# Kernel tuning notes

Measured on AMD Instinct MI355X. Metric: run time of the kernel, lower is better.

## Reference

```python
import jax, jax.numpy as jnp
import numpy as np

IH, IW = 14, 14
NUM_HEADS = 16
HEAD_DIMS = 32
INP_DIMS = 512
B = 128


def make_relative_position_index(ih, iw):
    coords = np.stack(np.meshgrid(np.arange(ih), np.arange(iw), indexing='ij'))  # [2, ih, iw]
    cf = coords.reshape(2, -1)  # [2, n]
    rel = cf[:, :, None] - cf[:, None, :]  # [2, n, n]
    rel = rel.transpose(1, 2, 0)  # [n, n, 2]
    rel[:, :, 0] += ih - 1
    rel[:, :, 1] += iw - 1
    rel[:, :, 0] *= 2 * iw - 1
    return rel.sum(-1).astype(np.int64)  # [n, n]


def setup_inputs() -> dict:
    key = jax.random.key(0)
    k1, k2, k3, k4, k5 = jax.random.split(key, 5)
    n = IH * IW
    inner = NUM_HEADS * HEAD_DIMS
    x = jax.random.normal(k1, (B, n, INP_DIMS), dtype=jnp.float32)
    qkv_w = jax.random.normal(k2, (INP_DIMS, 3 * inner), dtype=jnp.float32) * 0.02
    rel_bias_table = jax.random.normal(k3, ((2 * IH - 1) * (2 * IW - 1), NUM_HEADS), dtype=jnp.float32) * 0.02
    proj_w = jax.random.normal(k4, (inner, INP_DIMS), dtype=jnp.float32) * 0.02
    proj_b = jax.random.normal(k5, (INP_DIMS,), dtype=jnp.float32) * 0.02
    rel_pos_index = jnp.asarray(make_relative_position_index(IH, IW))
    return {"x": x, "qkv_w": qkv_w, "rel_bias_table": rel_bias_table,
            "proj_w": proj_w, "proj_b": proj_b, "rel_pos_index": rel_pos_index}


def reference(x, qkv_w, rel_bias_table, proj_w, proj_b, rel_pos_index):
    b, n, c = x.shape
    h, hd = NUM_HEADS, HEAD_DIMS
    scale = (INP_DIMS // NUM_HEADS) ** (-0.5)
    qkv = x @ qkv_w  # [b, n, 3*h*hd]
    qkv = qkv.reshape(b, n, 3, h, hd).transpose(2, 0, 3, 1, 4)  # [3, b, h, n, hd]
    q, k, v = qkv[0] * scale, qkv[1], qkv[2]
    attn = jnp.einsum('bhqd,bhkd->bhqk', q, k)  # [b, h, n, n]
    # gather relative position bias: [n*n, h] -> [h, n, n]
    bias = rel_bias_table[rel_pos_index.reshape(-1)].reshape(n, n, h).transpose(2, 0, 1)
    attn = jax.nn.softmax(attn + bias[None], axis=-1)
    out = jnp.einsum('bhqk,bhkd->bhqd', attn, v)  # [b, h, n, hd]
    out = out.transpose(0, 2, 1, 3).reshape(b, n, h * hd)
    return out @ proj_w + proj_b
```

## Files before the change

kernel.cpp:

```cpp
#include <hip/hip_runtime.h>

#define NTOK 196
#define QPAD 208
#define KP 208
#define PSTR 232
#define VKP 208

typedef __attribute__((ext_vector_type(8))) short short8;
typedef __attribute__((ext_vector_type(4))) short short4_t;
typedef __attribute__((ext_vector_type(4))) float float4_t;

__device__ __forceinline__ short f2bf(float f) {
  unsigned u = __float_as_uint(f);
  u = (u + 0x7fffu + ((u >> 16) & 1u)) >> 16;
  return (short)u;
}

__global__ __launch_bounds__(256) void fill_kernel(float* __restrict__ out,
                                                   int n) {
  int i = blockIdx.x * 256 + threadIdx.x;
  if (i < n) out[i] = 1000.0f;
}

__device__ __forceinline__ void transpose_body(const float* __restrict__ in,
                                               short* __restrict__ out, int R,
                                               int C, int bx, int by,
                                               float (*tile)[65]) {
  int c0 = bx * 64, r0 = by * 64;
  int tc = threadIdx.x & 63, tr = threadIdx.x >> 6;
#pragma unroll
  for (int s = 0; s < 16; s++) {
    int r = s * 4 + tr;
    tile[r][tc] = in[(r0 + r) * C + c0 + tc];
  }
  __syncthreads();
#pragma unroll
  for (int s = 0; s < 16; s++) {
    int i = s * 4 + tr;
    out[(c0 + i) * R + r0 + tc] = f2bf(tile[tc][i]);
  }
}

__global__ __launch_bounds__(256) void prep_kernel(
    const float* __restrict__ qkv_w, const float* __restrict__ proj_w,
    const float* __restrict__ table, const int* __restrict__ rpi,
    const float* __restrict__ x, short* __restrict__ wt1,
    short* __restrict__ wt2, float* __restrict__ bias, short* __restrict__ vb,
    short* __restrict__ xb, int do_vpad) {
  __shared__ float tile[64][65];
  int blk = blockIdx.x;
  if (blk < 192) {
    transpose_body(qkv_w, wt1, 512, 1536, blk % 24, blk / 24, tile);
  } else if (blk < 256) {
    int i = blk - 192;
    transpose_body(proj_w, wt2, 512, 512, i % 8, i / 8, tile);
  } else if (blk < 2960) {
    int idx = (blk - 256) * 256 + threadIdx.x;
    int h = idx / (QPAD * KP);
    int rem = idx % (QPAD * KP);
    int q = rem / KP, k = rem % KP;
    float v = 0.f;
    if (q < NTOK && k < NTOK)
      v = table[rpi[q * NTOK + k] * 16 + h] * 1.4426950408889634f;
    bias[idx] = v;
  } else if (blk < 3728) {
    if (do_vpad) {
      int i = (blk - 2960) * 256 + threadIdx.x;
      int row = i / 3, g = i - 3 * (i / 3);
      short4_t z = {0, 0, 0, 0};
      *(short4_t*)&vb[row * VKP + 196 + g * 4] = z;
    }
  } else {
    int i = ((blk - 3728) * 256 + threadIdx.x) * 8;
    float4_t a = *(const float4_t*)&x[i];
    float4_t b = *(const float4_t*)&x[i + 4];
    short8 v;
    v[0] = f2bf(a[0]); v[1] = f2bf(a[1]); v[2] = f2bf(a[2]); v[3] = f2bf(a[3]);
    v[4] = f2bf(b[0]); v[5] = f2bf(b[1]); v[6] = f2bf(b[2]); v[7] = f2bf(b[3]);
    *(short8*)&xb[i] = v;
  }
}

__device__ __forceinline__ void gemm_tile(const short* __restrict__ A,
                                          const short* __restrict__ B, int K,
                                          int m0, int n0, short (*As)[72],
                                          short (*Bs)[72], float4_t acc[4][4]) {
  int tid = threadIdx.x;
  int lane = tid & 63, wave = tid >> 6;
  int quad = lane >> 4, l16 = lane & 15;
  int wm = (wave >> 1) * 64, wn = (wave & 1) * 64;
  int srow = tid >> 3, scol = (tid & 7) * 8;
  for (int k0 = 0; k0 < K; k0 += 64) {
#pragma unroll
    for (int i = 0; i < 4; i++) {
      int r = srow + i * 32;
      *(short8*)&As[r][scol] = *(const short8*)&A[(m0 + r) * K + k0 + scol];
      *(short8*)&Bs[r][scol] = *(const short8*)&B[(n0 + r) * K + k0 + scol];
    }
    __syncthreads();
#pragma unroll
    for (int ks = 0; ks < 2; ks++) {
      short8 af[4], bfr[4];
#pragma unroll
      for (int i = 0; i < 4; i++) {
        af[i] = *(short8*)&As[wm + i * 16 + l16][ks * 32 + quad * 8];
        bfr[i] = *(short8*)&Bs[wn + i * 16 + l16][ks * 32 + quad * 8];
      }
#pragma unroll
      for (int mi = 0; mi < 4; mi++)
#pragma unroll
        for (int ni = 0; ni < 4; ni++)
          acc[mi][ni] = __builtin_amdgcn_mfma_f32_16x16x32_bf16(
              af[mi], bfr[ni], acc[mi][ni], 0, 0, 0);
    }
    __syncthreads();
  }
}

__global__ __launch_bounds__(256) void qkv_gemm(
    const short* __restrict__ xb, const short* __restrict__ wt1,
    short* __restrict__ qb, short* __restrict__ kb, short* __restrict__ vb) {
  __shared__ __align__(16) short As[128][72];
  __shared__ __align__(16) short Bs[128][72];
  float4_t acc[4][4];
  float4_t z = {0.f, 0.f, 0.f, 0.f};
#pragma unroll
  for (int i = 0; i < 4; i++)
#pragma unroll
    for (int j = 0; j < 4; j++) acc[i][j] = z;
  int lin = blockIdx.x + blockIdx.y * 12;
  int xcd = lin & 7, loc = lin >> 3;
  int nl = xcd * 294 + loc;
  int bx = nl % 12, by = nl / 12;
  int m0 = by * 128, n0 = bx * 128;
  gemm_tile(xb, wt1, 512, m0, n0, As, Bs, acc);
  int lane = threadIdx.x & 63, wave = threadIdx.x >> 6;
  int quad = lane >> 4, l16 = lane & 15;
  int wm = (wave >> 1) * 64, wn = (wave & 1) * 64;
  const float qscale = 0.17677669529663687f * 1.4426950408889634f;
#pragma unroll
  for (int mi = 0; mi < 4; mi++)
#pragma unroll
    for (int ni = 0; ni < 4; ni++) {
      int colg = n0 + wn + ni * 16 + l16;
      int s = colg >> 9, rem = colg & 511;
      int h = rem >> 5, d = rem & 31;
      int rowg0 = m0 + wm + mi * 16 + quad * 4;
      if (s == 2) {
        int b = rowg0 / NTOK, nt = rowg0 - b * NTOK;
        short4_t v4;
        v4[0] = f2bf(acc[mi][ni][0]);
        v4[1] = f2bf(acc[mi][ni][1]);
        v4[2] = f2bf(acc[mi][ni][2]);
        v4[3] = f2bf(acc[mi][ni][3]);
        *(short4_t*)&vb[((b * 16 + h) * 32 + d) * VKP + nt] = v4;
      } else {
#pragma unroll
        for (int r = 0; r < 4; r++) {
          int rowg = rowg0 + r;
          int b = rowg / NTOK, n = rowg - b * NTOK;
          int off = ((b * 16 + h) * QPAD + n) * 32 + d;
          if (s == 0)
            qb[off] = f2bf(acc[mi][ni][r] * qscale);
          else
            kb[off] = f2bf(acc[mi][ni][r]);
        }
      }
    }
}

__global__ __launch_bounds__(256) void attn_kernel(
    const short* __restrict__ qb, const short* __restrict__ kb,
    const short* __restrict__ vb, const float* __restrict__ bias,
    short* __restrict__ aout) {
  __shared__ __align__(16) short vT[32][PSTR];
  __shared__ __align__(16) short P[4][16][PSTR];
  int bh = blockIdx.x, b = bh >> 4, h = bh & 15;
  int tid = threadIdx.x, wave = tid >> 6, lane = tid & 63;
  int quad = lane >> 4, l16 = lane & 15;
  int base_row = b * NTOK;
  const short* vsrc = vb + bh * 32 * VKP;
  for (int i = tid; i < 32 * 26; i += 256) {
    int d = i / 26, c = (i - d * 26) * 8;
    *(short8*)&vT[d][c] = *(const short8*)&vsrc[d * VKP + c];
  }
  short8 z8 = {0, 0, 0, 0, 0, 0, 0, 0};
  if (tid < 96) {
    int d = tid / 3, c = 208 + (tid - d * 3) * 8;
    *(short8*)&vT[d][c] = z8;
  }
  __syncthreads();
  short8 kfr[13];
#pragma unroll
  for (int kt = 0; kt < 13; kt++)
    kfr[kt] = *(const short8*)&kb[(bh * QPAD + kt * 16 + l16) * 32 + quad * 8];
  float4_t z4 = {0.f, 0.f, 0.f, 0.f};
  for (int i2 = 0; i2 < 4; i2++) {
    bool active = (i2 < 3) || (wave == 0);
    if (!active) break;
    int qt = (i2 < 3) ? (wave + 4 * i2) : 12;
    int qr0 = qt * 16;
    short8 qf = *(const short8*)&qb[(bh * QPAD + qr0 + l16) * 32 + quad * 8];
    float4_t s[13];
#pragma unroll
    for (int kt = 0; kt < 13; kt++)
      s[kt] = __builtin_amdgcn_mfma_f32_16x16x32_bf16(qf, kfr[kt], z4, 0, 0, 0);
    const float* brow = bias + (h * QPAD + qr0 + quad * 4) * KP;
#pragma unroll
    for (int kt = 0; kt < 13; kt++) {
      int col = kt * 16 + l16;
#pragma unroll
      for (int r = 0; r < 4; r++) s[kt][r] += brow[r * KP + col];
    }
    if (l16 >= 4) {
#pragma unroll
      for (int r = 0; r < 4; r++) s[12][r] = -1e30f;
    }
    float invr[4];
#pragma unroll
    for (int r = 0; r < 4; r++) {
      float m = s[0][r];
#pragma unroll
      for (int kt = 1; kt < 13; kt++) m = fmaxf(m, s[kt][r]);
      m = fmaxf(m, __shfl_xor(m, 8, 16));
      m = fmaxf(m, __shfl_xor(m, 4, 16));
      m = fmaxf(m, __shfl_xor(m, 2, 16));
      m = fmaxf(m, __shfl_xor(m, 1, 16));
      float sum = 0.f;
#pragma unroll
      for (int kt = 0; kt < 13; kt++) {
        float p = exp2f(s[kt][r] - m);
        s[kt][r] = p;
        sum += p;
      }
      sum += __shfl_xor(sum, 8, 16);
      sum += __shfl_xor(sum, 4, 16);
      sum += __shfl_xor(sum, 2, 16);
      sum += __shfl_xor(sum, 1, 16);
      invr[r] = 1.f / sum;
      short* prow = &P[wave][quad * 4 + r][0];
#pragma unroll
      for (int kt = 0; kt < 13; kt++)
        prow[kt * 16 + l16] = f2bf(s[kt][r]);
      prow[208 + l16] = 0;
    }
    float4_t o0 = z4, o1 = z4;
#pragma unroll
    for (int kt = 0; kt < 7; kt++) {
      short8 pf = *(short8*)&P[wave][l16][kt * 32 + quad * 8];
      short8 vf0 = *(short8*)&vT[l16][kt * 32 + quad * 8];
      short8 vf1 = *(short8*)&vT[16 + l16][kt * 32 + quad * 8];
      o0 = __builtin_amdgcn_mfma_f32_16x16x32_bf16(pf, vf0, o0, 0, 0, 0);
      o1 = __builtin_amdgcn_mfma_f32_16x16x32_bf16(pf, vf1, o1, 0, 0, 0);
    }
#pragma unroll
    for (int r = 0; r < 4; r++) {
      int row = qr0 + quad * 4 + r;
      if (row < NTOK) {
        int off = (base_row + row) * 512 + h * 32;
        aout[off + l16] = f2bf(o0[r] * invr[r]);
        aout[off + 16 + l16] = f2bf(o1[r] * invr[r]);
      }
    }
  }
}

__global__ __launch_bounds__(256, 2) void fused_attn(
    const short* __restrict__ xb, const short* __restrict__ wt1,
    const float* __restrict__ bias, short* __restrict__ aout) {
  __shared__ __align__(16) short R1[64 * PSTR];
  __shared__ __align__(16) short R2[32 * PSTR];
  __shared__ __align__(16) short Qs[224][40];
  __shared__ __align__(16) short Ks[224][40];
  short(*As)[40] = (short(*)[40])R1;
  short(*P)[PSTR] = (short(*)[PSTR])R1;
  short(*Bs)[40] = (short(*)[40])R2;
  short(*vTs)[PSTR] = (short(*)[PSTR])R2;

  int bh = blockIdx.x, b = bh >> 4, h = bh & 15;
  int tid = threadIdx.x, wave = tid >> 6, lane = tid & 63;
  int quad = lane >> 4, l16 = lane & 15;
  int base_row = b * NTOK;

  float4_t z4 = {0.f, 0.f, 0.f, 0.f};
  float4_t acc[4][6];
#pragma unroll
  for (int i = 0; i < 4; i++)
#pragma unroll
    for (int n = 0; n < 6; n++) acc[i][n] = z4;

  int srow = tid >> 2, scol = (tid & 3) * 8;
  for (int k0 = 0; k0 < 512; k0 += 32) {
#pragma unroll
    for (int i = 0; i < 4; i++) {
      int r = srow + i * 64;
      if (r < 224) {
        int gr = base_row + r;
        if (gr > 25087) gr = 25087;
        *(short8*)&As[r][scol] = *(const short8*)&xb[gr * 512 + k0 + scol];
      }
    }
#pragma unroll
    for (int i = 0; i < 2; i++) {
      int r = srow + i * 64;
      if (r < 96) {
        int sec = r >> 5, r32 = r & 31;
        *(short8*)&Bs[r][scol] =
            *(const short8*)&wt1[(sec * 512 + h * 32 + r32) * 512 + k0 + scol];
      }
    }
    __syncthreads();
    short8 af[4], bfv[6];
#pragma unroll
    for (int i = 0; i < 4; i++) {
      int mt = (i < 3) ? (wave + 4 * i) : (12 + (wave & 1));
      af[i] = *(short8*)&As[mt * 16 + l16][quad * 8];
    }
#pragma unroll
    for (int n = 0; n < 6; n++) bfv[n] = *(short8*)&Bs[n * 16 + l16][quad * 8];
#pragma unroll
    for (int i = 0; i < 4; i++)
#pragma unroll
      for (int n = 0; n < 6; n++)
        acc[i][n] = __builtin_amdgcn_mfma_f32_16x16x32_bf16(af[i], bfv[n],
                                                            acc[i][n], 0, 0, 0);
    __syncthreads();
  }
  const float qscale = 0.17677669529663687f * 1.4426950408889634f;
#pragma unroll
  for (int i = 0; i < 4; i++) {
    if (i == 3 && wave >= 2) break;
    int mt = (i < 3) ? (wave + 4 * i) : (12 + wave);
    int row0 = mt * 16 + quad * 4;
#pragma unroll
    for (int n = 0; n < 6; n++) {
      int c = n * 16 + l16;
#pragma unroll
      for (int r = 0; r < 4; r++) {
        int row = row0 + r;
        float v = acc[i][n][r];
        if (c < 32)
          Qs[row][c] = f2bf(v * qscale);
        else if (c < 64)
          Ks[row][c - 32] = f2bf(v);
        else
          vTs[c - 64][row] = f2bf(v);
      }
    }
  }
  __syncthreads();
  for (int i2 = 0; i2 < 4; i2++) {
    bool active = (i2 < 3) || (wave == 0);
    int qt = (i2 < 3) ? (wave + 4 * i2) : 12;
    int qr0 = qt * 16;
    if (active) {
      short8 qf = *(short8*)&Qs[qr0 + l16][quad * 8];
      float4_t s[13];
#pragma unroll
      for (int kt = 0; kt < 13; kt++) {
        short8 kf = *(short8*)&Ks[kt * 16 + l16][quad * 8];
        s[kt] = __builtin_amdgcn_mfma_f32_16x16x32_bf16(qf, kf, z4, 0, 0, 0);
      }
      const float* brow = bias + (h * QPAD + qr0 + quad * 4) * KP;
#pragma unroll
      for (int kt = 0; kt < 13; kt++) {
        int col = kt * 16 + l16;
#pragma unroll
        for (int r = 0; r < 4; r++) s[kt][r] += brow[r * KP + col];
      }
      if (l16 >= 4) {
#pragma unroll
        for (int r = 0; r < 4; r++) s[12][r] = -1e30f;
      }
      int prow_base = wave * 16 + quad * 4;
#pragma unroll
      for (int r = 0; r < 4; r++) {
        float m = s[0][r];
#pragma unroll
        for (int kt = 1; kt < 13; kt++) m = fmaxf(m, s[kt][r]);
        m = fmaxf(m, __shfl_xor(m, 8, 16));
        m = fmaxf(m, __shfl_xor(m, 4, 16));
        m = fmaxf(m, __shfl_xor(m, 2, 16));
        m = fmaxf(m, __shfl_xor(m, 1, 16));
        float sum = 0.f;
#pragma unroll
        for (int kt = 0; kt < 13; kt++) {
          float p = exp2f(s[kt][r] - m);
          s[kt][r] = p;
          sum += p;
        }
        sum += __shfl_xor(sum, 8, 16);
        sum += __shfl_xor(sum, 4, 16);
        sum += __shfl_xor(sum, 2, 16);
        sum += __shfl_xor(sum, 1, 16);
        float inv = 1.f / sum;
        short* prow = &P[prow_base + r][0];
#pragma unroll
        for (int kt = 0; kt < 13; kt++)
          prow[kt * 16 + l16] = f2bf(s[kt][r] * inv);
        prow[208 + l16] = 0;
      }
    }
    __syncthreads();
    if (active) {
      float4_t o0 = z4, o1 = z4;
#pragma unroll
      for (int kt = 0; kt < 7; kt++) {
        short8 pf = *(short8*)&P[wave * 16 + l16][kt * 32 + quad * 8];
        short8 vf0 = *(short8*)&vTs[l16][kt * 32 + quad * 8];
        short8 vf1 = *(short8*)&vTs[16 + l16][kt * 32 + quad * 8];
        o0 = __builtin_amdgcn_mfma_f32_16x16x32_bf16(pf, vf0, o0, 0, 0, 0);
        o1 = __builtin_amdgcn_mfma_f32_16x16x32_bf16(pf, vf1, o1, 0, 0, 0);
      }
#pragma unroll
      for (int r = 0; r < 4; r++) {
        int row = qr0 + quad * 4 + r;
        if (row < NTOK) {
          int off = (base_row + row) * 512 + h * 32;
          aout[off + l16] = f2bf(o0[r]);
          aout[off + 16 + l16] = f2bf(o1[r]);
        }
      }
    }
    __syncthreads();
  }
}

__global__ __launch_bounds__(256) void proj_gemm(
    const short* __restrict__ a, const short* __restrict__ wt,
    const float* __restrict__ pb, float* __restrict__ out) {
  __shared__ __align__(16) short As[128][72];
  __shared__ __align__(16) short Bs[128][72];
  float4_t acc[4][4];
  float4_t z = {0.f, 0.f, 0.f, 0.f};
#pragma unroll
  for (int i = 0; i < 4; i++)
#pragma unroll
    for (int j = 0; j < 4; j++) acc[i][j] = z;
  int lin = blockIdx.x + blockIdx.y * 4;
  int xcd = lin & 7, loc = lin >> 3;
  int nl = xcd * 98 + loc;
  int bx = nl % 4, by = nl / 4;
  int m0 = by * 128, n0 = bx * 128;
  gemm_tile(a, wt, 512, m0, n0, As, Bs, acc);
  int lane = threadIdx.x & 63, wave = threadIdx.x >> 6;
  int quad = lane >> 4, l16 = lane & 15;
  int wm = (wave >> 1) * 64, wn = (wave & 1) * 64;
#pragma unroll
  for (int mi = 0; mi < 4; mi++)
#pragma unroll
    for (int ni = 0; ni < 4; ni++) {
      int colg = n0 + wn + ni * 16 + l16;
      float bv = pb[colg];
#pragma unroll
      for (int r = 0; r < 4; r++) {
        int rowg = m0 + wm + mi * 16 + quad * 4 + r;
        out[rowg * 512 + colg] = acc[mi][ni][r] + bv;
      }
    }
}

extern "C" void kernel_launch(void* const* d_in, const int* in_sizes, int n_in,
                              void* d_out, int out_size, void* d_ws,
                              size_t ws_size, hipStream_t stream) {
  const float* x = (const float*)d_in[0];
  const float* qkv_w = (const float*)d_in[1];
  const float* table = (const float*)d_in[2];
  const float* proj_w = (const float*)d_in[3];
  const float* proj_b = (const float*)d_in[4];
  const int* rpi = (const int*)d_in[5];
  float* out = (float*)d_out;

  char* w = (char*)d_ws;
  short* wt1 = (short*)(w);
  short* wt2 = (short*)(w + 1572864);
  float* bias = (float*)(w + 2097152);
  short* xb = (short*)(w + 4866048);
  short* qb = (short*)(w + 30556160);
  short* kb = (short*)(w + 57819136);
  short* vb = (short*)(w + 85082112);
  const size_t NEEDED_SPLIT = 112345088;
  const size_t NEEDED_FUSED = 30556160 + 25690112;

  int split = ws_size >= NEEDED_SPLIT;
  if (ws_size >= NEEDED_FUSED) {
    prep_kernel<<<10000, 256, 0, stream>>>(qkv_w, proj_w, table, rpi, x, wt1,
                                           wt2, bias, vb, xb, split);
  }
  if (split) {
    short* aout = xb;
    qkv_gemm<<<dim3(12, 196), 256, 0, stream>>>(xb, wt1, qb, kb, vb);
    attn_kernel<<<2048, 256, 0, stream>>>(qb, kb, vb, bias, aout);
    proj_gemm<<<dim3(4, 196), 256, 0, stream>>>(aout, wt2, proj_b, out);
  } else if (ws_size >= NEEDED_FUSED) {
    short* aout = (short*)(w + 30556160);
    fused_attn<<<2048, 256, 0, stream>>>(xb, wt1, bias, aout);
    proj_gemm<<<dim3(4, 196), 256, 0, stream>>>(aout, wt2, proj_b, out);
  } else {
    fill_kernel<<<(out_size + 255) / 256, 256, 0, stream>>>(out, out_size);
  }
}
```

Before: 271.7 us.

## Store relative-position bias in MFMA fragment order and feed it as accumulator

The precomputed bias table is laid out in the per-lane MFMA 16x16 accumulator fragment order, so each lane loads one contiguous float4 per key tile. That value is passed as the C operand of the MFMA instead of zero, which removes the separate strided scalar bias loads and adds. In one kernel the K fragments are now loaded inside the loop rather than held in 13 preloaded registers. This lowers register pressure but repeats the K loads for every query tile.

```diff
diff --git a/kernel.cpp b/kernel.cpp
--- a/kernel.cpp
+++ b/kernel.cpp
@@ -56,9 +56,15 @@
     transpose_body(proj_w, wt2, 512, 512, i % 8, i / 8, tile);
   } else if (blk < 2960) {
     int idx = (blk - 256) * 256 + threadIdx.x;
-    int h = idx / (QPAD * KP);
-    int rem = idx % (QPAD * KP);
-    int q = rem / KP, k = rem % KP;
+    int h = idx / 43264;
+    int rem = idx - h * 43264;
+    int qt = rem / 3328;
+    int rem2 = rem - qt * 3328;
+    int kt = rem2 >> 8;
+    int rem3 = rem2 & 255;
+    int lane = rem3 >> 2, r = rem3 & 3;
+    int q = qt * 16 + (lane >> 4) * 4 + r;
+    int k = kt * 16 + (lane & 15);
     float v = 0.f;
     if (q < NTOK && k < NTOK)
       v = table[rpi[q * NTOK + k] * 16 + h] * 1.4426950408889634f;
@@ -190,10 +196,7 @@
     *(short8*)&vT[d][c] = z8;
   }
   __syncthreads();
-  short8 kfr[13];
-#pragma unroll
-  for (int kt = 0; kt < 13; kt++)
-    kfr[kt] = *(const short8*)&kb[(bh * QPAD + kt * 16 + l16) * 32 + quad * 8];
+  const float4_t* bfrag = (const float4_t*)bias;
   float4_t z4 = {0.f, 0.f, 0.f, 0.f};
   for (int i2 = 0; i2 < 4; i2++) {
     bool active = (i2 < 3) || (wave == 0);
@@ -201,16 +204,14 @@
     int qt = (i2 < 3) ? (wave + 4 * i2) : 12;
     int qr0 = qt * 16;
     short8 qf = *(const short8*)&qb[(bh * QPAD + qr0 + l16) * 32 + quad * 8];
+    const float4_t* bq = bfrag + (h * 13 + qt) * 13 * 64 + lane;
     float4_t s[13];
 #pragma unroll
-    for (int kt = 0; kt < 13; kt++)
-      s[kt] = __builtin_amdgcn_mfma_f32_16x16x32_bf16(qf, kfr[kt], z4, 0, 0, 0);
-    const float* brow = bias + (h * QPAD + qr0 + quad * 4) * KP;
-#pragma unroll
     for (int kt = 0; kt < 13; kt++) {
-      int col = kt * 16 + l16;
-#pragma unroll
-      for (int r = 0; r < 4; r++) s[kt][r] += brow[r * KP + col];
+      short8 kf =
+          *(const short8*)&kb[(bh * QPAD + kt * 16 + l16) * 32 + quad * 8];
+      s[kt] =
+          __builtin_amdgcn_mfma_f32_16x16x32_bf16(qf, kf, bq[kt * 64], 0, 0, 0);
     }
     if (l16 >= 4) {
 #pragma unroll
@@ -355,18 +356,14 @@
     int qr0 = qt * 16;
     if (active) {
       short8 qf = *(short8*)&Qs[qr0 + l16][quad * 8];
+      const float4_t* bq =
+          (const float4_t*)bias + (h * 13 + qt) * 13 * 64 + lane;
       float4_t s[13];
 #pragma unroll
       for (int kt = 0; kt < 13; kt++) {
         short8 kf = *(short8*)&Ks[kt * 16 + l16][quad * 8];
-        s[kt] = __builtin_amdgcn_mfma_f32_16x16x32_bf16(qf, kf, z4, 0, 0, 0);
-      }
-      const float* brow = bias + (h * QPAD + qr0 + quad * 4) * KP;
-#pragma unroll
-      for (int kt = 0; kt < 13; kt++) {
-        int col = kt * 16 + l16;
-#pragma unroll
-        for (int r = 0; r < 4; r++) s[kt][r] += brow[r * KP + col];
+        s[kt] = __builtin_amdgcn_mfma_f32_16x16x32_bf16(qf, kf, bq[kt * 64], 0,
+                                                        0, 0);
       }
       if (l16 >= 4) {
 #pragma unroll
```

After: 265.6 us. 1.02x faster.
